# Kernel tuning notes

Hardware: AMD Instinct MI355X
Metric: run time of the kernel (lower is better)

## Reference

```python
import jax, jax.numpy as jnp
import numpy as np

N, E, L, D, ED, M = 100000, 1600000, 4, 64, 16, 128
BN_EPS = 1e-5


def _bn(x, w, b):
    # BatchNorm1d in training mode: biased batch stats over the node dim
    m = x.mean(0)
    v = jnp.mean((x - m) ** 2, axis=0)
    return (x - m) * jax.lax.rsqrt(v + BN_EPS) * w + b


def _leaky(x):
    return jnp.where(x > 0, x, 0.01 * x)  # torch LeakyReLU default slope


def setup_inputs() -> dict:
    key = jax.random.key(0)
    ks = jax.random.split(key, 8)
    s = 0.05
    return {
        "x": jax.random.normal(ks[0], (N, D), jnp.float32),
        "edge_index": jax.random.randint(ks[1], (2, E), 0, N, jnp.int32),
        "edge_attr": jax.random.normal(ks[2], (E, ED), jnp.float32),
        "bn_pre_w": jnp.ones((L, D), jnp.float32),
        "bn_pre_b": jnp.zeros((L, D), jnp.float32),
        "edge_lin_w": jax.random.normal(ks[3], (L, D, ED), jnp.float32) * s,
        "edge_lin_b": jnp.zeros((L, D), jnp.float32),
        "lin1_w": jax.random.normal(ks[4], (L, D, D), jnp.float32) * s,
        "lin1_b": jnp.zeros((L, D), jnp.float32),
        "bn_mid_w": jnp.ones((L, D), jnp.float32),
        "bn_mid_b": jnp.zeros((L, D), jnp.float32),
        "lin2_w": jax.random.normal(ks[5], (L, D, D), jnp.float32) * s,
        "lin2_b": jnp.zeros((L, D), jnp.float32),
        "eps": jnp.zeros((L,), jnp.float32),
        "cls1_w": jax.random.normal(ks[6], (M, D), jnp.float32) * s,
        "cls1_b": jnp.zeros((M,), jnp.float32),
        "cls_bn_w": jnp.ones((M,), jnp.float32),
        "cls_bn_b": jnp.zeros((M,), jnp.float32),
        "cls2_w": jax.random.normal(ks[7], (1, M), jnp.float32) * s,
        "cls2_b": jnp.zeros((1,), jnp.float32),
    }


def reference(x, edge_index, edge_attr, bn_pre_w, bn_pre_b, edge_lin_w, edge_lin_b,
              lin1_w, lin1_b, bn_mid_w, bn_mid_b, lin2_w, lin2_b, eps,
              cls1_w, cls1_b, cls_bn_w, cls_bn_b, cls2_w, cls2_b):
    src, dst = edge_index[0], edge_index[1]
    h = x
    for i in range(L):  # fixed, small layer count
        hn = _bn(h, bn_pre_w[i], bn_pre_b[i])
        hi = hn if i == 0 else _leaky(hn)
        # GINEConv: msg = relu(x_src + Lin(edge_attr)); sum-aggregate at dst
        e = edge_attr @ edge_lin_w[i].T + edge_lin_b[i]            # [E, D]
        msg = jax.nn.relu(hi[src] + e)                              # gather [E, D]
        aggr = jax.ops.segment_sum(msg, dst, num_segments=N)        # scatter [N, D]
        z = (1.0 + eps[i]) * hi + aggr
        # nn: Linear -> BN -> LeakyReLU -> Linear
        z = z @ lin1_w[i].T + lin1_b[i]
        z = _leaky(_bn(z, bn_mid_w[i], bn_mid_b[i]))
        z = z @ lin2_w[i].T + lin2_b[i]
        h = z if i == 0 else h + z  # residual (skipped on first layer)
    y = _leaky(_bn(h @ cls1_w.T + cls1_b, cls_bn_w, cls_bn_b))
    y = y @ cls2_w.T + cls2_b
    return y.reshape(-1)  # torch.flatten -> [N]
```

## Files before the change

kernel.cpp:

```cpp
#include <hip/hip_runtime.h>
#include <hip/hip_bf16.h>

constexpr int GN = 100000;
constexpr int GE = 1600000;
constexpr float FN = 100000.0f;
constexpr float BN_EPS = 1e-5f;

typedef __attribute__((ext_vector_type(8))) short bf16x8;
typedef __attribute__((ext_vector_type(4))) float f32x4;
typedef __bf16 bfp2 __attribute__((ext_vector_type(2)));

#if __has_builtin(__builtin_amdgcn_fdot2_f32_bf16)
#define HAVE_DOT2 1
#else
#define HAVE_DOT2 0
#endif

__device__ __forceinline__ unsigned packbf2(float a, float b) {
    __hip_bfloat162 h = __float22bfloat162_rn(float2{a, b});
    union { __hip_bfloat162 h2; unsigned u; } cv;
    cv.h2 = h;
    return cv.u;
}

__device__ __forceinline__ unsigned short bf16rn(float f) {
    unsigned u = __builtin_bit_cast(unsigned, f);
    unsigned r = (u + 0x7FFF + ((u >> 16) & 1)) >> 16;
    return (unsigned short)r;
}

__device__ __forceinline__ float bflo(unsigned u) {
    return __builtin_bit_cast(float, u << 16);
}
__device__ __forceinline__ float bfhi(unsigned u) {
    return __builtin_bit_cast(float, u & 0xFFFF0000u);
}
__device__ __forceinline__ float bfu16(unsigned short u) {
    return __builtin_bit_cast(float, (unsigned)u << 16);
}


__global__ __launch_bounds__(256) void hist_kernel(const int* __restrict__ dst,
                                                   int* __restrict__ deg) {
    for (int i = blockIdx.x * blockDim.x + threadIdx.x; i < GE; i += gridDim.x * blockDim.x)
        atomicAdd(&deg[dst[i]], 1);
}

__global__ __launch_bounds__(256) void bsum_kernel(const int* __restrict__ deg,
                                                   int* __restrict__ bsum,
                                                   const float* __restrict__ l1w,
                                                   const float* __restrict__ l2w,
                                                   const float* __restrict__ c1w,
                                                   unsigned short* __restrict__ wb) {
    int b = blockIdx.x;
    int i0 = b * 1024 + threadIdx.x * 4;
    int s = 0;
#pragma unroll
    for (int k = 0; k < 4; ++k) {
        int i = i0 + k;
        if (i < GN) s += deg[i];
    }
    for (int o = 32; o >= 1; o >>= 1) s += __shfl_down(s, o, 64);
    __shared__ int ws[4];
    if ((threadIdx.x & 63) == 0) ws[threadIdx.x >> 6] = s;
    __syncthreads();
    if (threadIdx.x == 0) bsum[b] = ws[0] + ws[1] + ws[2] + ws[3];
    for (int i = b * 256 + threadIdx.x; i < 40960; i += gridDim.x * 256) {
        float v;
        if (i < 16384) v = l1w[i];
        else if (i < 32768) v = l2w[i - 16384];
        else v = c1w[i - 32768];
        wb[i] = bf16rn(v);
    }
}

__global__ void bscan_kernel(const int* __restrict__ bsum, int* __restrict__ bbase,
                             int* __restrict__ offEnd, int nb) {
    int t = threadIdx.x;
    int carry = 0;
    for (int base = 0; base < nb; base += 64) {
        int v = (base + t < nb) ? bsum[base + t] : 0;
        int incl = v;
        for (int o = 1; o < 64; o <<= 1) {
            int u = __shfl_up(incl, o, 64);
            if (t >= o) incl += u;
        }
        if (base + t < nb) bbase[base + t] = carry + incl - v;
        carry += __shfl(incl, 63, 64);
    }
    if (t == 0) offEnd[0] = carry;
}

__global__ __launch_bounds__(256) void bscatter_kernel(int* __restrict__ deg,
                                                       const int* __restrict__ bbase,
                                                       int* __restrict__ off) {
    int b = blockIdx.x;
    int t = threadIdx.x;
    int i0 = b * 1024 + t * 4;
    int v[4];
    int s = 0;
#pragma unroll
    for (int k = 0; k < 4; ++k) {
        int i = i0 + k;
        v[k] = (i < GN) ? deg[i] : 0;
        s += v[k];
    }
    int incl = s;
    int lane = t & 63;
    for (int o = 1; o < 64; o <<= 1) {
        int u = __shfl_up(incl, o, 64);
        if (lane >= o) incl += u;
    }
    __shared__ int wsum[4];
    if (lane == 63) wsum[t >> 6] = incl;
    __syncthreads();
    int w = t >> 6;
    int wb = 0;
#pragma unroll
    for (int k = 0; k < 4; ++k)
        if (k < w) wb += wsum[k];
    int ex = bbase[b] + wb + incl - s;
#pragma unroll
    for (int k = 0; k < 4; ++k) {
        int i = i0 + k;
        if (i < GN) { off[i] = ex; deg[i] = ex; }
        ex += v[k];
    }
}

__global__ __launch_bounds__(256) void scatter_perm_kernel(
    const int* __restrict__ dst,
    int* __restrict__ cursor,
    int* __restrict__ perm,
    float* __restrict__ zeroBuf) {
    if (blockIdx.x == 0 && threadIdx.x < 128) zeroBuf[threadIdx.x] = 0.f;
    for (int i = blockIdx.x * blockDim.x + threadIdx.x; i < GE; i += gridDim.x * blockDim.x) {
        int pos = atomicAdd(&cursor[dst[i]], 1);
        perm[pos] = i;
    }
}

__global__ __launch_bounds__(256) void gather_sorted_kernel(
    const int* __restrict__ perm, const int* __restrict__ src,
    const float4* __restrict__ attr,
    int* __restrict__ srcS, uint2* __restrict__ attrS2) {
    int q = threadIdx.x & 3;
    int row0 = blockIdx.x * 64 + (threadIdx.x >> 2);
    int stride = gridDim.x * 64;
    for (int p = row0; p < GE; p += stride) {
        int eid = perm[p];
        float4 a = attr[(size_t)eid * 4 + q];
        uint2 u;
        u.x = packbf2(a.x, a.y);
        u.y = packbf2(a.z, a.w);
        attrS2[(size_t)p * 4 + q] = u;
        if (q == 0) srcS[p] = src[eid];
    }
}


__global__ __launch_bounds__(256) void col_stats64(const float* __restrict__ in,
                                                   float* __restrict__ sum,
                                                   float* __restrict__ sq,
                                                   unsigned short* __restrict__ outb) {
    int c = threadIdx.x & 63;
    int lr = threadIdx.x >> 6;
    float s = 0.f, q = 0.f;
    for (int r = blockIdx.x * 4 + lr; r < GN; r += gridDim.x * 4) {
        float v = in[(size_t)r * 64 + c];
        s += v;
        q += v * v;
        outb[(size_t)r * 64 + c] = bf16rn(v);
    }
    __shared__ float S[256];
    S[threadIdx.x] = s;
    __syncthreads();
    if (threadIdx.x < 64) {
        float a = S[threadIdx.x] + S[threadIdx.x + 64] + S[threadIdx.x + 128] + S[threadIdx.x + 192];
        atomicAdd(&sum[threadIdx.x], a);
    }
    __syncthreads();
    S[threadIdx.x] = q;
    __syncthreads();
    if (threadIdx.x < 64) {
        float a = S[threadIdx.x] + S[threadIdx.x + 64] + S[threadIdx.x + 128] + S[threadIdx.x + 192];
        atomicAdd(&sq[threadIdx.x], a);
    }
}


#if HAVE_DOT2
__device__ __forceinline__ float edot(uint4 a, uint4 b, const bfp2* __restrict__ wq,
                                      float e) {
    e = __builtin_amdgcn_fdot2_f32_bf16(__builtin_bit_cast(bfp2, a.x), wq[0], e, false);
    e = __builtin_amdgcn_fdot2_f32_bf16(__builtin_bit_cast(bfp2, a.y), wq[1], e, false);
    e = __builtin_amdgcn_fdot2_f32_bf16(__builtin_bit_cast(bfp2, a.z), wq[2], e, false);
    e = __builtin_amdgcn_fdot2_f32_bf16(__builtin_bit_cast(bfp2, a.w), wq[3], e, false);
    e = __builtin_amdgcn_fdot2_f32_bf16(__builtin_bit_cast(bfp2, b.x), wq[4], e, false);
    e = __builtin_amdgcn_fdot2_f32_bf16(__builtin_bit_cast(bfp2, b.y), wq[5], e, false);
    e = __builtin_amdgcn_fdot2_f32_bf16(__builtin_bit_cast(bfp2, b.z), wq[6], e, false);
    e = __builtin_amdgcn_fdot2_f32_bf16(__builtin_bit_cast(bfp2, b.w), wq[7], e, false);
    return e;
}
#else
__device__ __forceinline__ float edot(uint4 a, uint4 b, const float* __restrict__ w,
                                      float e) {
    e = fmaf(bflo(a.x), w[0], e);  e = fmaf(bfhi(a.x), w[1], e);
    e = fmaf(bflo(a.y), w[2], e);  e = fmaf(bfhi(a.y), w[3], e);
    e = fmaf(bflo(a.z), w[4], e);  e = fmaf(bfhi(a.z), w[5], e);
    e = fmaf(bflo(a.w), w[6], e);  e = fmaf(bfhi(a.w), w[7], e);
    e = fmaf(bflo(b.x), w[8], e);  e = fmaf(bfhi(b.x), w[9], e);
    e = fmaf(bflo(b.y), w[10], e); e = fmaf(bfhi(b.y), w[11], e);
    e = fmaf(bflo(b.z), w[12], e); e = fmaf(bfhi(b.z), w[13], e);
    e = fmaf(bflo(b.w), w[14], e); e = fmaf(bfhi(b.w), w[15], e);
    return e;
}
#endif

__global__ __launch_bounds__(256) void aggregate_kernel(
    const float* __restrict__ h,
    const unsigned short* __restrict__ hb,
    const float* __restrict__ sumv, const float* __restrict__ sqv,
    const float* __restrict__ bnw, const float* __restrict__ bnb,
    int leaky,
    const int* __restrict__ off,
    const int* __restrict__ srcS,
    const unsigned* __restrict__ attrS,
    const float* __restrict__ Wle, const float* __restrict__ ble,
    const float* __restrict__ epsArr, int layer,
    unsigned short* __restrict__ zb,
    float* __restrict__ zeroBuf) {
    if (blockIdx.x == 0 && threadIdx.x < 128) zeroBuf[threadIdx.x] = 0.f;
    const int d = threadIdx.x & 63;
    const int node = __builtin_amdgcn_readfirstlane(blockIdx.x * 4 + (threadIdx.x >> 6));

    float mean = sumv[d] / FN;
    float var = sqv[d] / FN - mean * mean;
    float cA = rsqrtf(var + BN_EPS) * bnw[d];
    float cB = bnb[d] - mean * cA;

#if HAVE_DOT2
    bfp2 wq[8];
#pragma unroll
    for (int k = 0; k < 8; ++k) {
        float2 t = *(const float2*)(Wle + d * 16 + k * 2);
        bfp2 v = {(__bf16)t.x, (__bf16)t.y};
        wq[k] = v;
    }
#else
    float wq[16];
#pragma unroll
    for (int k = 0; k < 16; k += 4) {
        float4 t = *(const float4*)(Wle + d * 16 + k);
        wq[k] = t.x; wq[k + 1] = t.y; wq[k + 2] = t.z; wq[k + 3] = t.w;
    }
#endif
    float be = ble[d];
    float epsv = 1.0f + epsArr[layer];

    int p0 = off[node], p1 = off[node + 1];
    float hv = h[(size_t)node * 64 + d];

    float acc = 0.0f;
    int p = p0;
    int pfull = p0 + ((p1 - p0) & ~7);
    for (; p < pfull; p += 8) {
        int idx[8];
#pragma unroll
        for (int j = 0; j < 8; ++j) idx[j] = srcS[p + j];
        float g[8];
#pragma unroll
        for (int j = 0; j < 8; ++j)
            g[j] = bfu16(hb[(((unsigned)idx[j]) << 6) + d]);
#pragma unroll
        for (int j = 0; j < 8; ++j) {
            const uint4* ar = (const uint4*)(attrS + (size_t)(p + j) * 8);
            float e = edot(ar[0], ar[1], wq, be);
            float gg = g[j] * cA + cB;
            if (leaky) gg = fmaxf(gg, 0.01f * gg);
            acc += fmaxf(gg + e, 0.f);
        }
    }
    for (; p < p1; p += 4) {
        int idx[4];
#pragma unroll
        for (int j = 0; j < 4; ++j) {
            int q = p + j;
            if (q > p1 - 1) q = p1 - 1;
            idx[j] = srcS[q];
        }
        float g[4];
#pragma unroll
        for (int j = 0; j < 4; ++j)
            g[j] = bfu16(hb[(((unsigned)idx[j]) << 6) + d]);
#pragma unroll
        for (int j = 0; j < 4; ++j) {
            int q = p + j;
            if (q > p1 - 1) q = p1 - 1;
            const uint4* ar = (const uint4*)(attrS + (size_t)q * 8);
            float e = edot(ar[0], ar[1], wq, be);
            float gg = g[j] * cA + cB;
            if (leaky) gg = fmaxf(gg, 0.01f * gg);
            float m = fmaxf(gg + e, 0.f);
            acc += (p + j < p1) ? m : 0.f;
        }
    }
    hv = hv * cA + cB;
    if (leaky) hv = fmaxf(hv, 0.01f * hv);
    zb[(size_t)node * 64 + d] = bf16rn(epsv * hv + acc);
}


template <bool BN_IN, bool ABF16, bool STATS, bool RESID, bool BF16OUT, bool F32OUT>
__global__ __launch_bounds__(256) void gemm_mfma(
    const float* __restrict__ srcf, const unsigned short* __restrict__ srcb, int src_ld,
    const unsigned short* __restrict__ Wb,
    const float* __restrict__ bias,
    float* __restrict__ dst, int dst_ld,
    unsigned short* __restrict__ dstb, int dstb_ld,
    const float* __restrict__ resid,
    const float* __restrict__ statsInSum, const float* __restrict__ statsInSq,
    const float* __restrict__ bnw, const float* __restrict__ bnb,
    float* __restrict__ statsOutSum, float* __restrict__ statsOutSq,
    float* __restrict__ zeroBuf, int zeroN) {
    __shared__ float cA[64], cB[64];
    __shared__ float sS[64], sQ[64];
    int tid = threadIdx.x;
    if (zeroBuf && blockIdx.x == 0 && blockIdx.y == 0 && tid < zeroN) zeroBuf[tid] = 0.f;
    int c0 = blockIdx.y * 64;

    if (BN_IN) {
        if (tid < 64) {
            float m = statsInSum[tid] / FN;
            float v = statsInSq[tid] / FN - m * m;
            float a = rsqrtf(v + BN_EPS) * bnw[tid];
            cA[tid] = a;
            cB[tid] = bnb[tid] - m * a;
        }
        __syncthreads();
    }

    int w = tid >> 6, lane = tid & 63;
    int n16 = lane & 15, quad = lane >> 4;

    bf16x8 bfr[4][2];
#pragma unroll
    for (int t = 0; t < 4; ++t) {
        int col = c0 + t * 16 + n16;
        const unsigned short* bsrc = Wb + (size_t)col * 64 + quad * 8;
#pragma unroll
        for (int kk = 0; kk < 2; ++kk)
            bfr[t][kk] = *(const bf16x8*)(bsrc + kk * 32);
    }

    float ls[4] = {0.f, 0.f, 0.f, 0.f}, lq[4] = {0.f, 0.f, 0.f, 0.f};
    constexpr int NT = (GN + 63) / 64;
    for (int tile = blockIdx.x; tile < NT; tile += gridDim.x) {
        int r0 = tile * 64;
        int arow = r0 + w * 16 + n16;
        int arc = arow < GN ? arow : 0;

        bf16x8 afr[2];
        if (ABF16) {
            const unsigned short* asrc = srcb + (size_t)arc * src_ld + quad * 8;
#pragma unroll
            for (int kk = 0; kk < 2; ++kk)
                afr[kk] = *(const bf16x8*)(asrc + kk * 32);
        } else {
            const float* asrc = srcf + (size_t)arc * src_ld + quad * 8;
#pragma unroll
            for (int kk = 0; kk < 2; ++kk) {
                const float4* p = (const float4*)(asrc + kk * 32);
                float4 x0 = p[0], x1 = p[1];
                float av[8] = {x0.x, x0.y, x0.z, x0.w, x1.x, x1.y, x1.z, x1.w};
                if (BN_IN) {
                    int kb = quad * 8 + kk * 32;
#pragma unroll
                    for (int j = 0; j < 8; ++j) {
                        float t = av[j] * cA[kb + j] + cB[kb + j];
                        av[j] = fmaxf(t, 0.01f * t);
                    }
                }
                uint4 fu;
                fu.x = packbf2(av[0], av[1]); fu.y = packbf2(av[2], av[3]);
                fu.z = packbf2(av[4], av[5]); fu.w = packbf2(av[6], av[7]);
                afr[kk] = __builtin_bit_cast(bf16x8, fu);
            }
        }

        f32x4 acc[4] = {{0.f, 0.f, 0.f, 0.f}, {0.f, 0.f, 0.f, 0.f},
                        {0.f, 0.f, 0.f, 0.f}, {0.f, 0.f, 0.f, 0.f}};
#pragma unroll
        for (int t = 0; t < 4; ++t) {
            acc[t] = __builtin_amdgcn_mfma_f32_16x16x32_bf16(afr[0], bfr[t][0], acc[t], 0, 0, 0);
            acc[t] = __builtin_amdgcn_mfma_f32_16x16x32_bf16(afr[1], bfr[t][1], acc[t], 0, 0, 0);
        }

#pragma unroll
        for (int t = 0; t < 4; ++t) {
            int col = c0 + t * 16 + n16;
            float bv = bias[col];
#pragma unroll
            for (int r = 0; r < 4; ++r) {
                int row = r0 + w * 16 + quad * 4 + r;
                if (row < GN) {
                    float o = acc[t][r] + bv;
                    if (RESID) o += resid[(size_t)row * dst_ld + col];
                    if (F32OUT) dst[(size_t)row * dst_ld + col] = o;
                    if (BF16OUT) dstb[(size_t)row * dstb_ld + col] = bf16rn(o);
                    if (STATS) { ls[t] += o; lq[t] += o * o; }
                }
            }
        }
    }

    if (STATS) {
        if (tid < 64) { sS[tid] = 0.f; sQ[tid] = 0.f; }
        __syncthreads();
#pragma unroll
        for (int t = 0; t < 4; ++t) {
            float s = ls[t], q = lq[t];
            s += __shfl_down(s, 16, 64); s += __shfl_down(s, 32, 64);
            q += __shfl_down(q, 16, 64); q += __shfl_down(q, 32, 64);
            if (lane < 16) {
                atomicAdd(&sS[t * 16 + n16], s);
                atomicAdd(&sQ[t * 16 + n16], q);
            }
        }
        __syncthreads();
        if (tid < 64) {
            atomicAdd(&statsOutSum[c0 + tid], sS[tid]);
            atomicAdd(&statsOutSq[c0 + tid], sQ[tid]);
        }
    }
}


__global__ __launch_bounds__(256) void cls2_kernel(
    const unsigned short* __restrict__ y1b,
    const float* __restrict__ sum, const float* __restrict__ sq,
    const float* __restrict__ bnw, const float* __restrict__ bnb,
    const float* __restrict__ w2, const float* __restrict__ b2,
    float* __restrict__ out) {
    int node = blockIdx.x * 4 + (threadIdx.x >> 6);
    int d = threadIdx.x & 63;
    if (node >= GN) return;
    float partial = 0.f;
#pragma unroll
    for (int hh = 0; hh < 2; ++hh) {
        int c = d + hh * 64;
        float m = sum[c] / FN;
        float var = sq[c] / FN - m * m;
        float a = rsqrtf(var + BN_EPS) * bnw[c];
        float v = bfu16(y1b[(size_t)node * 128 + c]);
        v = v * a + (bnb[c] - m * a);
        v = fmaxf(v, 0.01f * v);
        partial += v * w2[c];
    }
    for (int o = 32; o >= 1; o >>= 1) partial += __shfl_down(partial, o, 64);
    if (d == 0) out[node] = partial + b2[0];
}


extern "C" void kernel_launch(void* const* d_in, const int* in_sizes, int n_in,
                              void* d_out, int out_size, void* d_ws, size_t ws_size,
                              hipStream_t stream) {
    (void)in_sizes; (void)n_in; (void)out_size; (void)ws_size;
    const float* x    = (const float*)d_in[0];
    const int*   ei   = (const int*)d_in[1];
    const float* attr = (const float*)d_in[2];
    const float* bnpw = (const float*)d_in[3];
    const float* bnpb = (const float*)d_in[4];
    const float* elw  = (const float*)d_in[5];
    const float* elb  = (const float*)d_in[6];
    const float* l1w  = (const float*)d_in[7];
    const float* l1b  = (const float*)d_in[8];
    const float* bnmw = (const float*)d_in[9];
    const float* bnmb = (const float*)d_in[10];
    const float* l2w  = (const float*)d_in[11];
    const float* l2b  = (const float*)d_in[12];
    const float* epsA = (const float*)d_in[13];
    const float* c1w  = (const float*)d_in[14];
    const float* c1b  = (const float*)d_in[15];
    const float* cbw  = (const float*)d_in[16];
    const float* cbb  = (const float*)d_in[17];
    const float* c2w  = (const float*)d_in[18];
    const float* c2b  = (const float*)d_in[19];
    const int* srcArr = ei;
    const int* dstArr = ei + GE;

    char* base = (char*)d_ws;
    size_t ofs = 0;
    auto alloc = [&](size_t bytes) {
        void* p = base + ofs;
        ofs = (ofs + bytes + 1023) & ~(size_t)1023;
        return p;
    };
    int* off              = (int*)alloc((size_t)(GN + 1) * 4);
    int* cursor           = (int*)alloc((size_t)GN * 4);
    int* src_sorted       = (int*)alloc((size_t)GE * 4);
    unsigned* attr_sorted = (unsigned*)alloc((size_t)GE * 32);
    unsigned short* wbf   = (unsigned short*)alloc(40960 * 2);
    int* bsum   = (int*)alloc(1024);
    int* bbase  = (int*)alloc(1024);
    float* stP0 = (float*)alloc(512);
    float* stP1 = (float*)alloc(512);
    float* stM  = (float*)alloc(512);
    float* stC  = (float*)alloc(1024);
    float* h = (float*)alloc((size_t)GN * 256);
    float* z = (float*)alloc((size_t)GN * 256);
    unsigned short* zb = (unsigned short*)alloc((size_t)GN * 128);
    unsigned short* xb = (unsigned short*)alloc((size_t)GN * 128);
    unsigned short* hb = (unsigned short*)alloc((size_t)GN * 128);
    unsigned short* y1b = (unsigned short*)attr_sorted;
    int* perm = (int*)z;

    constexpr int NB = (GN + 1023) / 1024;
    float* stP[2] = {stP0, stP1};

    hipMemsetAsync(cursor, 0, (size_t)GN * 4, stream);
    hist_kernel<<<2048, 256, 0, stream>>>(dstArr, cursor);
    bsum_kernel<<<NB, 256, 0, stream>>>(cursor, bsum, l1w, l2w, c1w, wbf);
    bscan_kernel<<<1, 64, 0, stream>>>(bsum, bbase, off + GN, NB);
    bscatter_kernel<<<NB, 256, 0, stream>>>(cursor, bbase, off);
    scatter_perm_kernel<<<2048, 256, 0, stream>>>(dstArr, cursor, perm, stP0);
    gather_sorted_kernel<<<4096, 256, 0, stream>>>(perm, srcArr, (const float4*)attr,
                                                   src_sorted, (uint2*)attr_sorted);

    col_stats64<<<512, 256, 0, stream>>>(x, stP0, stP0 + 64, xb);

    const float* hsrc = x;
    const unsigned short* hbsrc = xb;
    dim3 gg(782, 1);
    for (int i = 0; i < 4; ++i) {
        float* sIn = stP[i & 1];
        float* sNext = stP[(i + 1) & 1];
        aggregate_kernel<<<25000, 256, 0, stream>>>(
            hsrc, hbsrc, sIn, sIn + 64, bnpw + i * 64, bnpb + i * 64, (i > 0) ? 1 : 0,
            off, src_sorted, attr_sorted, elw + i * 1024, elb + i * 64, epsA, i,
            zb, stM);
        gemm_mfma<false, true, true, false, false, true><<<gg, 256, 0, stream>>>(
            nullptr, zb, 64, wbf + i * 4096, l1b + i * 64, z, 64, nullptr, 0, nullptr,
            nullptr, nullptr, nullptr, nullptr, stM, stM + 64,
            (i == 3) ? stC : sNext, (i == 3) ? 256 : 128);
        if (i == 0)
            gemm_mfma<true, false, true, false, true, true><<<gg, 256, 0, stream>>>(
                z, nullptr, 64, wbf + 16384 + i * 4096, l2b + i * 64, h, 64, hb, 64,
                nullptr, stM, stM + 64, bnmw + i * 64, bnmb + i * 64,
                sNext, sNext + 64, nullptr, 0);
        else if (i < 3)
            gemm_mfma<true, false, true, true, true, true><<<gg, 256, 0, stream>>>(
                z, nullptr, 64, wbf + 16384 + i * 4096, l2b + i * 64, h, 64, hb, 64,
                h, stM, stM + 64, bnmw + i * 64, bnmb + i * 64,
                sNext, sNext + 64, nullptr, 0);
        else
            gemm_mfma<true, false, false, true, true, true><<<gg, 256, 0, stream>>>(
                z, nullptr, 64, wbf + 16384 + i * 4096, l2b + i * 64, h, 64, hb, 64,
                h, stM, stM + 64, bnmw + i * 64, bnmb + i * 64,
                nullptr, nullptr, nullptr, 0);
        hsrc = h;
        hbsrc = hb;
    }

    dim3 gc(391, 2);
    gemm_mfma<false, true, true, false, true, false><<<gc, 256, 0, stream>>>(
        nullptr, hb, 64, wbf + 32768, c1b, nullptr, 128, y1b, 128, nullptr,
        nullptr, nullptr, nullptr, nullptr, stC, stC + 128, nullptr, 0);
    cls2_kernel<<<25000, 256, 0, stream>>>(y1b, stC, stC + 128, cbw, cbb, c2w, c2b,
                                           (float*)d_out);
}
```

Measured before the change: 1.099 ms.

## Replace per-edge CSR scatter with two-pass bucketed binning by destination

The edge sort by destination becomes a two-level counting sort. Edges are first binned into 128-node buckets, split into 8 sub-streams to reduce atomic contention, and written as (edge, src, dst) records. A per-bucket pass then places each edge using shared-memory cursors and gathers its attributes. This replaces random global atomics and scattered perm writes with mostly local bucket work, at the cost of an extra 16-byte record pass and one more scan kernel. The placement order within each node now depends on atomic timing, so it is non-deterministic.

New measurement: 1.156 ms. 1.05x slower.

```diff
diff --git a/kernel.cpp b/kernel.cpp
--- a/kernel.cpp
+++ b/kernel.cpp
@@ -5,6 +5,9 @@
 constexpr int GE = 1600000;
 constexpr float FN = 100000.0f;
 constexpr float BN_EPS = 1e-5f;
+
+constexpr int NBUK = (GN + 127) / 128;
+constexpr int NSTRM = NBUK * 8;
 
 typedef __attribute__((ext_vector_type(8))) short bf16x8;
 typedef __attribute__((ext_vector_type(4))) float f32x4;
@@ -41,9 +44,14 @@
 
 
 __global__ __launch_bounds__(256) void hist_kernel(const int* __restrict__ dst,
-                                                   int* __restrict__ deg) {
-    for (int i = blockIdx.x * blockDim.x + threadIdx.x; i < GE; i += gridDim.x * blockDim.x)
-        atomicAdd(&deg[dst[i]], 1);
+                                                   int* __restrict__ deg,
+                                                   int* __restrict__ bxc) {
+    int s = blockIdx.x & 7;
+    for (int i = blockIdx.x * blockDim.x + threadIdx.x; i < GE; i += gridDim.x * blockDim.x) {
+        int dv = dst[i];
+        atomicAdd(&deg[dv], 1);
+        atomicAdd(&bxc[((dv >> 7) << 3) + s], 1);
+    }
 }
 
 __global__ __launch_bounds__(256) void bsum_kernel(const int* __restrict__ deg,
@@ -123,38 +131,93 @@
 #pragma unroll
     for (int k = 0; k < 4; ++k) {
         int i = i0 + k;
-        if (i < GN) { off[i] = ex; deg[i] = ex; }
+        if (i < GN) off[i] = ex;
         ex += v[k];
     }
 }
 
-__global__ __launch_bounds__(256) void scatter_perm_kernel(
-    const int* __restrict__ dst,
-    int* __restrict__ cursor,
-    int* __restrict__ perm,
-    float* __restrict__ zeroBuf) {
-    if (blockIdx.x == 0 && threadIdx.x < 128) zeroBuf[threadIdx.x] = 0.f;
+__global__ __launch_bounds__(256) void scan_bxc_kernel(const int* __restrict__ bxc,
+                                                       int* __restrict__ bbase2,
+                                                       int* __restrict__ bcur,
+                                                       float* __restrict__ zeroBuf) {
+    int t = threadIdx.x;
+    if (t < 128) zeroBuf[t] = 0.f;
+    constexpr int PT = (NSTRM + 255) / 256;
+    int v[PT];
+    int s = 0;
+#pragma unroll
+    for (int k = 0; k < PT; ++k) {
+        int idx = t * PT + k;
+        int x = (idx < NSTRM) ? bxc[idx] : 0;
+        v[k] = x;
+        s += x;
+    }
+    int lane = t & 63, w = t >> 6;
+    int incl = s;
+    for (int o = 1; o < 64; o <<= 1) {
+        int u = __shfl_up(incl, o, 64);
+        if (lane >= o) incl += u;
+    }
+    __shared__ int ws[4];
+    if (lane == 63) ws[w] = incl;
+    __syncthreads();
+    int wb = 0;
+#pragma unroll
+    for (int k = 0; k < 4; ++k)
+        if (k < w) wb += ws[k];
+    int ex = wb + incl - s;
+#pragma unroll
+    for (int k = 0; k < PT; ++k) {
+        int idx = t * PT + k;
+        if (idx < NSTRM) { bbase2[idx] = ex; bcur[idx] = ex; }
+        ex += v[k];
+    }
+    if (t == 255) bbase2[NSTRM] = GE;
+}
+
+__global__ __launch_bounds__(256) void binA_kernel(const int* __restrict__ src,
+                                                   const int* __restrict__ dst,
+                                                   int* __restrict__ bcur,
+                                                   uint4* __restrict__ pairs) {
+    int s = blockIdx.x & 7;
     for (int i = blockIdx.x * blockDim.x + threadIdx.x; i < GE; i += gridDim.x * blockDim.x) {
-        int pos = atomicAdd(&cursor[dst[i]], 1);
-        perm[pos] = i;
-    }
-}
-
-__global__ __launch_bounds__(256) void gather_sorted_kernel(
-    const int* __restrict__ perm, const int* __restrict__ src,
-    const float4* __restrict__ attr,
-    int* __restrict__ srcS, uint2* __restrict__ attrS2) {
-    int q = threadIdx.x & 3;
-    int row0 = blockIdx.x * 64 + (threadIdx.x >> 2);
-    int stride = gridDim.x * 64;
-    for (int p = row0; p < GE; p += stride) {
-        int eid = perm[p];
-        float4 a = attr[(size_t)eid * 4 + q];
+        int dv = dst[i];
+        int sv = src[i];
+        int slot = atomicAdd(&bcur[((dv >> 7) << 3) + s], 1);
+        uint4 pr;
+        pr.x = (unsigned)i; pr.y = (unsigned)sv; pr.z = (unsigned)dv; pr.w = 0u;
+        pairs[slot] = pr;
+    }
+}
+
+__global__ __launch_bounds__(256) void binB_kernel(const uint4* __restrict__ pairs,
+                                                   const int* __restrict__ bbase2,
+                                                   const int* __restrict__ off,
+                                                   const float4* __restrict__ attr,
+                                                   int* __restrict__ srcS,
+                                                   uint2* __restrict__ attrS2) {
+    __shared__ int cur[128];
+    int b = blockIdx.x;
+    int t = threadIdx.x;
+    if (t < 128) {
+        int n = (b << 7) + t;
+        cur[t] = (n < GN) ? off[n] : 0;
+    }
+    __syncthreads();
+    int s0 = bbase2[b << 3];
+    int s1 = bbase2[(b << 3) + 8];
+    int q = t & 3, g = t >> 2, lane = t & 63;
+    for (int p = s0 + g; p < s1; p += 64) {
+        uint4 pr = pairs[p];
+        int pos = 0;
+        if (q == 0) pos = atomicAdd(&cur[pr.z & 127], 1);
+        pos = __shfl(pos, lane & ~3, 64);
+        float4 a = attr[(size_t)pr.x * 4 + q];
         uint2 u;
         u.x = packbf2(a.x, a.y);
         u.y = packbf2(a.z, a.w);
-        attrS2[(size_t)p * 4 + q] = u;
-        if (q == 0) srcS[p] = src[eid];
+        attrS2[(size_t)pos * 4 + q] = u;
+        if (q == 0) srcS[pos] = (int)pr.y;
     }
 }
 
@@ -498,6 +561,9 @@
     };
     int* off              = (int*)alloc((size_t)(GN + 1) * 4);
     int* cursor           = (int*)alloc((size_t)GN * 4);
+    int* bxc              = (int*)alloc((size_t)(NSTRM + 1) * 4);
+    int* bbase2           = (int*)alloc((size_t)(NSTRM + 1) * 4);
+    int* bcur             = (int*)alloc((size_t)NSTRM * 4);
     int* src_sorted       = (int*)alloc((size_t)GE * 4);
     unsigned* attr_sorted = (unsigned*)alloc((size_t)GE * 32);
     unsigned short* wbf   = (unsigned short*)alloc(40960 * 2);
@@ -513,19 +579,21 @@
     unsigned short* xb = (unsigned short*)alloc((size_t)GN * 128);
     unsigned short* hb = (unsigned short*)alloc((size_t)GN * 128);
     unsigned short* y1b = (unsigned short*)attr_sorted;
-    int* perm = (int*)z;
+    uint4* pairs = (uint4*)z;
 
     constexpr int NB = (GN + 1023) / 1024;
     float* stP[2] = {stP0, stP1};
 
-    hipMemsetAsync(cursor, 0, (size_t)GN * 4, stream);
-    hist_kernel<<<2048, 256, 0, stream>>>(dstArr, cursor);
+    size_t zlen = (size_t)((char*)bxc - (char*)cursor) + (size_t)(NSTRM + 1) * 4;
+    hipMemsetAsync(cursor, 0, zlen, stream);
+    hist_kernel<<<2048, 256, 0, stream>>>(dstArr, cursor, bxc);
     bsum_kernel<<<NB, 256, 0, stream>>>(cursor, bsum, l1w, l2w, c1w, wbf);
     bscan_kernel<<<1, 64, 0, stream>>>(bsum, bbase, off + GN, NB);
     bscatter_kernel<<<NB, 256, 0, stream>>>(cursor, bbase, off);
-    scatter_perm_kernel<<<2048, 256, 0, stream>>>(dstArr, cursor, perm, stP0);
-    gather_sorted_kernel<<<4096, 256, 0, stream>>>(perm, srcArr, (const float4*)attr,
-                                                   src_sorted, (uint2*)attr_sorted);
+    scan_bxc_kernel<<<1, 256, 0, stream>>>(bxc, bbase2, bcur, stP0);
+    binA_kernel<<<2048, 256, 0, stream>>>(srcArr, dstArr, bcur, pairs);
+    binB_kernel<<<NBUK, 256, 0, stream>>>(pairs, bbase2, off, (const float4*)attr,
+                                          src_sorted, (uint2*)attr_sorted);
 
     col_stats64<<<512, 256, 0, stream>>>(x, stP0, stP0 + 64, xb);
 
```

## Replace atomic counting sort of edges with two-pass LSD radix sort

Applied to the files above, without the earlier changes.

Replaces the global-atomic histogram and scatter that built the dst-sorted edge permutation with a two-pass LSD radix sort (8 low bits, then the high bits) using per-block LDS histograms, bin scans and a stable warp-ballot scatter. Row offsets come from a binary search over the sorted keys. The goal is to remove contended global atomics and random perm writes and to get a deterministic stable order. In exchange it adds more kernel launches, two passes over 8-byte pairs, and a serialized per-wave scatter loop with a __syncthreads on every wave step.

New measurement: 948.9 us. 1.16x faster.

```diff
diff --git a/kernel.cpp b/kernel.cpp
--- a/kernel.cpp
+++ b/kernel.cpp
@@ -5,6 +5,9 @@
 constexpr int GE = 1600000;
 constexpr float FN = 100000.0f;
 constexpr float BN_EPS = 1e-5f;
+
+constexpr int SB = 512;
+constexpr int TILE = (GE + SB - 1) / SB;
 
 typedef __attribute__((ext_vector_type(8))) short bf16x8;
 typedef __attribute__((ext_vector_type(4))) float f32x4;
@@ -39,33 +42,27 @@
     return __builtin_bit_cast(float, (unsigned)u << 16);
 }
 
-
-__global__ __launch_bounds__(256) void hist_kernel(const int* __restrict__ dst,
-                                                   int* __restrict__ deg) {
-    for (int i = blockIdx.x * blockDim.x + threadIdx.x; i < GE; i += gridDim.x * blockDim.x)
-        atomicAdd(&deg[dst[i]], 1);
-}
-
-__global__ __launch_bounds__(256) void bsum_kernel(const int* __restrict__ deg,
-                                                   int* __restrict__ bsum,
-                                                   const float* __restrict__ l1w,
-                                                   const float* __restrict__ l2w,
-                                                   const float* __restrict__ c1w,
-                                                   unsigned short* __restrict__ wb) {
-    int b = blockIdx.x;
-    int i0 = b * 1024 + threadIdx.x * 4;
-    int s = 0;
-#pragma unroll
-    for (int k = 0; k < 4; ++k) {
-        int i = i0 + k;
-        if (i < GN) s += deg[i];
-    }
-    for (int o = 32; o >= 1; o >>= 1) s += __shfl_down(s, o, 64);
-    __shared__ int ws[4];
-    if ((threadIdx.x & 63) == 0) ws[threadIdx.x >> 6] = s;
-    __syncthreads();
-    if (threadIdx.x == 0) bsum[b] = ws[0] + ws[1] + ws[2] + ws[3];
-    for (int i = b * 256 + threadIdx.x; i < 40960; i += gridDim.x * 256) {
+__device__ __forceinline__ int permb(int b) { return ((b & 7) << 6) | (b >> 3); }
+
+
+__global__ __launch_bounds__(256) void h1_kernel(const int* __restrict__ dst,
+                                                 int* __restrict__ hist1,
+                                                 const float* __restrict__ l1w,
+                                                 const float* __restrict__ l2w,
+                                                 const float* __restrict__ c1w,
+                                                 unsigned short* __restrict__ wb,
+                                                 float* __restrict__ zeroBuf) {
+    __shared__ int cnt[256];
+    int b = blockIdx.x, t = threadIdx.x;
+    if (b == 0 && t < 128) zeroBuf[t] = 0.f;
+    cnt[t] = 0;
+    __syncthreads();
+    int e0 = b * TILE, e1 = min(e0 + TILE, GE);
+    for (int i = e0 + t; i < e1; i += 256)
+        atomicAdd(&cnt[dst[i] & 255], 1);
+    __syncthreads();
+    hist1[t * SB + permb(b)] = cnt[t];
+    for (int i = b * 256 + t; i < 40960; i += SB * 256) {
         float v;
         if (i < 16384) v = l1w[i];
         else if (i < 32768) v = l2w[i - 16384];
@@ -74,81 +71,152 @@
     }
 }
 
-__global__ void bscan_kernel(const int* __restrict__ bsum, int* __restrict__ bbase,
-                             int* __restrict__ offEnd, int nb) {
-    int t = threadIdx.x;
-    int carry = 0;
-    for (int base = 0; base < nb; base += 64) {
-        int v = (base + t < nb) ? bsum[base + t] : 0;
-        int incl = v;
-        for (int o = 1; o < 64; o <<= 1) {
-            int u = __shfl_up(incl, o, 64);
-            if (t >= o) incl += u;
-        }
-        if (base + t < nb) bbase[base + t] = carry + incl - v;
-        carry += __shfl(incl, 63, 64);
-    }
-    if (t == 0) offEnd[0] = carry;
-}
-
-__global__ __launch_bounds__(256) void bscatter_kernel(int* __restrict__ deg,
-                                                       const int* __restrict__ bbase,
-                                                       int* __restrict__ off) {
-    int b = blockIdx.x;
-    int t = threadIdx.x;
-    int i0 = b * 1024 + t * 4;
-    int v[4];
-    int s = 0;
-#pragma unroll
-    for (int k = 0; k < 4; ++k) {
-        int i = i0 + k;
-        v[k] = (i < GN) ? deg[i] : 0;
-        s += v[k];
-    }
+__global__ __launch_bounds__(256) void s1_kernel(int* __restrict__ hist,
+                                                 int* __restrict__ binTot) {
+    int bin = blockIdx.x, t = threadIdx.x;
+    int v0 = hist[bin * SB + 2 * t], v1 = hist[bin * SB + 2 * t + 1];
+    int s = v0 + v1;
+    int lane = t & 63, w = t >> 6;
     int incl = s;
-    int lane = t & 63;
     for (int o = 1; o < 64; o <<= 1) {
         int u = __shfl_up(incl, o, 64);
         if (lane >= o) incl += u;
     }
-    __shared__ int wsum[4];
-    if (lane == 63) wsum[t >> 6] = incl;
-    __syncthreads();
-    int w = t >> 6;
+    __shared__ int ws_[4];
+    if (lane == 63) ws_[w] = incl;
+    __syncthreads();
     int wb = 0;
 #pragma unroll
     for (int k = 0; k < 4; ++k)
-        if (k < w) wb += wsum[k];
-    int ex = bbase[b] + wb + incl - s;
-#pragma unroll
-    for (int k = 0; k < 4; ++k) {
-        int i = i0 + k;
-        if (i < GN) { off[i] = ex; deg[i] = ex; }
-        ex += v[k];
-    }
-}
-
-__global__ __launch_bounds__(256) void scatter_perm_kernel(
-    const int* __restrict__ dst,
-    int* __restrict__ cursor,
-    int* __restrict__ perm,
-    float* __restrict__ zeroBuf) {
-    if (blockIdx.x == 0 && threadIdx.x < 128) zeroBuf[threadIdx.x] = 0.f;
-    for (int i = blockIdx.x * blockDim.x + threadIdx.x; i < GE; i += gridDim.x * blockDim.x) {
-        int pos = atomicAdd(&cursor[dst[i]], 1);
-        perm[pos] = i;
-    }
+        if (k < w) wb += ws_[k];
+    int ex = wb + incl - s;
+    hist[bin * SB + 2 * t] = ex;
+    hist[bin * SB + 2 * t + 1] = ex + v0;
+    if (t == 255) binTot[bin] = ex + s;
+}
+
+__global__ __launch_bounds__(256) void s2_kernel(int* __restrict__ a, int n) {
+    int t = threadIdx.x;
+    int v0 = (2 * t < n) ? a[2 * t] : 0;
+    int v1 = (2 * t + 1 < n) ? a[2 * t + 1] : 0;
+    int s = v0 + v1;
+    int lane = t & 63, w = t >> 6;
+    int incl = s;
+    for (int o = 1; o < 64; o <<= 1) {
+        int u = __shfl_up(incl, o, 64);
+        if (lane >= o) incl += u;
+    }
+    __shared__ int ws_[4];
+    if (lane == 63) ws_[w] = incl;
+    __syncthreads();
+    int wb = 0;
+#pragma unroll
+    for (int k = 0; k < 4; ++k)
+        if (k < w) wb += ws_[k];
+    int ex = wb + incl - s;
+    if (2 * t < n) a[2 * t] = ex;
+    if (2 * t + 1 < n) a[2 * t + 1] = ex + v0;
+}
+
+__global__ __launch_bounds__(256) void scat1_kernel(const int* __restrict__ dst,
+                                                    const int* __restrict__ hist1,
+                                                    const int* __restrict__ binBase1,
+                                                    uint2* __restrict__ out) {
+    __shared__ int base[256];
+    int b = blockIdx.x, t = threadIdx.x;
+    base[t] = hist1[t * SB + permb(b)] + binBase1[t];
+    __syncthreads();
+    int e0 = b * TILE, e1 = min(e0 + TILE, GE);
+    for (int i = e0 + t; i < e1; i += 256) {
+        int dv = dst[i];
+        int pos = atomicAdd(&base[dv & 255], 1);
+        uint2 pr;
+        pr.x = (unsigned)i;
+        pr.y = (unsigned)dv;
+        out[pos] = pr;
+    }
+}
+
+__global__ __launch_bounds__(256) void h2_kernel(const uint2* __restrict__ in,
+                                                 int* __restrict__ hist2) {
+    __shared__ int cnt[512];
+    int b = blockIdx.x, t = threadIdx.x;
+    int tp = permb(b);
+    cnt[t] = 0;
+    cnt[t + 256] = 0;
+    __syncthreads();
+    int e0 = tp * TILE, e1 = min(e0 + TILE, GE);
+    for (int i = e0 + t; i < e1; i += 256)
+        atomicAdd(&cnt[in[i].y >> 8], 1);
+    __syncthreads();
+    hist2[t * SB + tp] = cnt[t];
+    hist2[(t + 256) * SB + tp] = cnt[t + 256];
+}
+
+__global__ __launch_bounds__(256) void scat2_kernel(const uint2* __restrict__ in,
+                                                    const int* __restrict__ hist2,
+                                                    const int* __restrict__ binBase2,
+                                                    uint2* __restrict__ out) {
+    __shared__ int base[512];
+    int b = blockIdx.x, t = threadIdx.x;
+    int tp = permb(b);
+    base[t] = hist2[t * SB + tp] + binBase2[t];
+    base[t + 256] = hist2[(t + 256) * SB + tp] + binBase2[t + 256];
+    __syncthreads();
+    int e0 = tp * TILE, e1 = min(e0 + TILE, GE);
+    int lane = t & 63, w = t >> 6;
+    unsigned long long below = (1ull << lane) - 1ull;
+    if (lane == 63) below = ~0ull >> 1;
+    for (int r = e0; r < e1; r += 256) {
+        int i = r + t;
+        bool valid = (i < e1);
+        uint2 el;
+        el.x = 0u; el.y = 0u;
+        if (valid) el = in[i];
+        int bin = (int)(el.y >> 8);
+        unsigned long long m = __ballot(valid);
+#pragma unroll
+        for (int bb = 0; bb < 9; ++bb) {
+            unsigned long long bm = __ballot((bin >> bb) & 1);
+            m &= ((bin >> bb) & 1) ? bm : ~bm;
+        }
+        int rank = __popcll(m & below);
+        int cntm = __popcll(m);
+        bool leader = valid && ((m & below) == 0ull);
+#pragma unroll
+        for (int ws = 0; ws < 4; ++ws) {
+            if (w == ws && valid) {
+                int p0 = base[bin];
+                if (leader) base[bin] = p0 + cntm;
+                out[p0 + rank] = el;
+            }
+            __syncthreads();
+        }
+    }
+}
+
+__global__ __launch_bounds__(256) void off_kernel(const uint2* __restrict__ sorted,
+                                                  int* __restrict__ off) {
+    int n = blockIdx.x * 256 + threadIdx.x;
+    if (n > GN) return;
+    if (n == GN) { off[GN] = GE; return; }
+    int lo = 0, hi = GE;
+    while (lo < hi) {
+        int mid = (lo + hi) >> 1;
+        if ((int)sorted[mid].y < n) lo = mid + 1; else hi = mid;
+    }
+    off[n] = lo;
 }
 
 __global__ __launch_bounds__(256) void gather_sorted_kernel(
-    const int* __restrict__ perm, const int* __restrict__ src,
+    const uint2* __restrict__ sorted, const int* __restrict__ src,
     const float4* __restrict__ attr,
     int* __restrict__ srcS, uint2* __restrict__ attrS2) {
     int q = threadIdx.x & 3;
     int row0 = blockIdx.x * 64 + (threadIdx.x >> 2);
     int stride = gridDim.x * 64;
     for (int p = row0; p < GE; p += stride) {
-        int eid = perm[p];
+        int eid = (int)sorted[p].x;
         float4 a = attr[(size_t)eid * 4 + q];
         uint2 u;
         u.x = packbf2(a.x, a.y);
@@ -497,12 +565,13 @@
         return p;
     };
     int* off              = (int*)alloc((size_t)(GN + 1) * 4);
-    int* cursor           = (int*)alloc((size_t)GN * 4);
+    int* hist1            = (int*)alloc((size_t)256 * SB * 4);
+    int* hist2            = (int*)alloc((size_t)512 * SB * 4);
+    int* binTot1          = (int*)alloc(512 * 4);
+    int* binTot2          = (int*)alloc(512 * 4);
     int* src_sorted       = (int*)alloc((size_t)GE * 4);
     unsigned* attr_sorted = (unsigned*)alloc((size_t)GE * 32);
     unsigned short* wbf   = (unsigned short*)alloc(40960 * 2);
-    int* bsum   = (int*)alloc(1024);
-    int* bbase  = (int*)alloc(1024);
     float* stP0 = (float*)alloc(512);
     float* stP1 = (float*)alloc(512);
     float* stM  = (float*)alloc(512);
@@ -513,18 +582,21 @@
     unsigned short* xb = (unsigned short*)alloc((size_t)GN * 128);
     unsigned short* hb = (unsigned short*)alloc((size_t)GN * 128);
     unsigned short* y1b = (unsigned short*)attr_sorted;
-    int* perm = (int*)z;
-
-    constexpr int NB = (GN + 1023) / 1024;
+    uint2* pairsA = (uint2*)z;
+    uint2* pairsB = (uint2*)((char*)z + (size_t)GE * 8);
+
     float* stP[2] = {stP0, stP1};
 
-    hipMemsetAsync(cursor, 0, (size_t)GN * 4, stream);
-    hist_kernel<<<2048, 256, 0, stream>>>(dstArr, cursor);
-    bsum_kernel<<<NB, 256, 0, stream>>>(cursor, bsum, l1w, l2w, c1w, wbf);
-    bscan_kernel<<<1, 64, 0, stream>>>(bsum, bbase, off + GN, NB);
-    bscatter_kernel<<<NB, 256, 0, stream>>>(cursor, bbase, off);
-    scatter_perm_kernel<<<2048, 256, 0, stream>>>(dstArr, cursor, perm, stP0);
-    gather_sorted_kernel<<<4096, 256, 0, stream>>>(perm, srcArr, (const float4*)attr,
+    h1_kernel<<<SB, 256, 0, stream>>>(dstArr, hist1, l1w, l2w, c1w, wbf, stP0);
+    s1_kernel<<<256, 256, 0, stream>>>(hist1, binTot1);
+    s2_kernel<<<1, 256, 0, stream>>>(binTot1, 256);
+    scat1_kernel<<<SB, 256, 0, stream>>>(dstArr, hist1, binTot1, pairsA);
+    h2_kernel<<<SB, 256, 0, stream>>>(pairsA, hist2);
+    s1_kernel<<<512, 256, 0, stream>>>(hist2, binTot2);
+    s2_kernel<<<1, 256, 0, stream>>>(binTot2, 512);
+    scat2_kernel<<<SB, 256, 0, stream>>>(pairsA, hist2, binTot2, pairsB);
+    off_kernel<<<392, 256, 0, stream>>>(pairsB, off);
+    gather_sorted_kernel<<<4096, 256, 0, stream>>>(pairsB, srcArr, (const float4*)attr,
                                                    src_sorted, (uint2*)attr_sorted);
 
     col_stats64<<<512, 256, 0, stream>>>(x, stP0, stP0 + 64, xb);
```
